# Optimization experiments

Hardware: AMD Instinct MI355X
Metric: run time of the kernel (lower is better)

Reference implementation:

```python
import jax, jax.numpy as jnp
import numpy as np

MARGIN = 0.0
GAP = 0.4
N, D, C = 8192, 128, 10


def setup_inputs() -> dict:
    key = jax.random.key(0)
    k1, k2, k3 = jax.random.split(key, 3)
    inputs = jax.random.normal(k1, (N, D), dtype=jnp.float32)
    pred = jax.random.normal(k2, (N, C), dtype=jnp.float32)
    targets = jax.random.randint(k3, (N,), 0, C, dtype=jnp.int64)
    return {"inputs": inputs, "pred": pred, "targets": targets}


def reference(inputs, pred, targets):
    n = inputs.shape[0]
    # pairwise euclidean distances: ||xi||^2 + ||xj||^2 - 2 xi.xj, clamped + sqrt
    sq = jnp.sum(inputs * inputs, axis=1)                      # [n]
    dist = sq[:, None] + sq[None, :] - 2.0 * (inputs @ inputs.T)
    dist = jnp.sqrt(jnp.clip(dist, 1e-12))                     # [n, n]
    same = targets[:, None] == targets[None, :]                # [n, n] bool

    # confusion detection (original runs under no_grad)
    p = jax.nn.softmax(jax.lax.stop_gradient(pred), axis=1)
    val, top2 = jax.lax.top_k(p, 2)                            # [n,2]
    confuse = (val[:, 0] - val[:, 1] <= GAP) | (top2[:, 0] != targets)  # [n]

    # hard mining per row: hardest positive (max over same-class), hardest negative (min over diff-class)
    dist_ap = jnp.max(jnp.where(same, dist, -jnp.inf), axis=1)  # [n]
    dist_an = jnp.min(jnp.where(same, jnp.inf, dist), axis=1)   # [n]

    # MarginRankingLoss(margin=MARGIN) with y=1: mean(relu(-(an - ap) + margin)) over confused rows
    per_row = jnp.maximum(dist_ap - dist_an + MARGIN, 0.0)
    cnt = jnp.sum(confuse.astype(jnp.float32))
    loss = jnp.sum(jnp.where(confuse, per_row, 0.0)) / jnp.maximum(cnt, 1.0)
    return jnp.where(cnt > 0, loss, 0.0)
```

## Files before the change

### kernel.cpp

```cpp
#include <hip/hip_runtime.h>

#define NROWS 8192
#define DIMX  128
#define KB    192
#define KSEG  12
#define PTB   24576
#define NKS   3
#define NCLS  10
#define GAPV  0.4f
#define DEBIAS 504.03125f
#define SCL   (-0.0078125f)
#define RGR   256
#define NRG   (NROWS / RGR)
#define CHUNK 512
#define NCHUNK (NROWS / CHUNK)
#define NT    (CHUNK / 16)
#define PRW   32

typedef __attribute__((ext_vector_type(4))) int i32x4;

__device__ __forceinline__ int q8(float v) {
  int q = (int)rintf(16.f * v);
  return q > 127 ? 127 : (q < -127 ? -127 : q);
}
__device__ __forceinline__ int pk4(float4 v) {
  return (q8(v.x) & 255) | ((q8(v.y) & 255) << 8) |
         ((q8(v.z) & 255) << 16) | ((q8(v.w) & 255) << 24);
}

__global__ __launch_bounds__(256) void prep_k(const float* __restrict__ x,
                                              const int* __restrict__ tgt,
                                              const float* __restrict__ pred,
                                              char* __restrict__ xa,
                                              char* __restrict__ xbm,
                                              float* __restrict__ sq,
                                              int* __restrict__ conf,
                                              int* __restrict__ emin,
                                              int* __restrict__ emax,
                                              unsigned* __restrict__ ctrs) {
  __shared__ char  pan[8 * PRW * 16];
  __shared__ float ssq[PRW];
  const int tid = threadIdx.x;
  const int blk = blockIdx.x;
  if (blk == 0 && tid < 35) ctrs[tid] = 0u;

  {
    const int r32 = tid >> 3;
    const int sg  = tid & 7;
    const float4* xr = (const float4*)(x + (size_t)(blk * PRW + r32) * DIMX) + sg * 4;
    float ss = 0.f;
    i32x4 w;
    #pragma unroll
    for (int k = 0; k < 4; ++k) {
      const float4 v = xr[k];
      ss += v.x * v.x + v.y * v.y + v.z * v.z + v.w * v.w;
      w[k] = pk4(v);
    }
    *(i32x4*)&pan[(sg * PRW + r32) * 16] = w;
    ss += __shfl_xor(ss, 1, 64);
    ss += __shfl_xor(ss, 2, 64);
    ss += __shfl_xor(ss, 4, 64);
    if (sg == 0) ssq[r32] = ss;
  }
  __syncthreads();

  const int panel = blk >> 2;
  const int rbase = (blk & 3) * PRW;

  {
    const int kseg = tid >> 5;
    const int r32  = tid & 31;
    const i32x4 w = *(const i32x4*)&pan[(kseg * PRW + r32) * 16];
    const size_t off = (size_t)panel * PTB + (size_t)kseg * 2048 + (size_t)(rbase + r32) * 16;
    *(i32x4*)(xa + off)  = w;
    *(i32x4*)(xbm + off) = w;
  }

  if (tid < PRW) {
    const int row = blk * PRW + tid;
    const float s = ssq[tid];
    const int cls = tgt[row];
    const int K  = min((int)rintf(128.f * s), 32385);
    const int t2 = min(K / 127, 254);
    const int b1 = t2 < 127 ? t2 : 127;
    const int b2 = t2 - b1;
    const int rr = min(K - 127 * t2, 126);

    i32x4 a8 = {0,0,0,0}, a9 = {0,0,0,0}, a10 = {0,0,0,0}, z = {0,0,0,0};
    i32x4 b8 = {0,0,0,0}, b9 = {0,0,0,0}, b10 = {0,0,0,0};
    if (cls < 4)      { a8[cls]      = 0x7F7F7F7F; b8[cls]      = (int)0x81818181; }
    else if (cls < 8) { a9[cls - 4]  = 0x7F7F7F7F; b9[cls - 4]  = (int)0x81818181; }
    else              { a10[cls - 8] = 0x7F7F7F7F; b10[cls - 8] = (int)0x81818181; }
    a10[2] = 0x00017F7F;
    b10[2] = ((-b1) & 255) | (((-b2) & 255) << 8) | (((-rr) & 255) << 16);

    char* pa = xa  + (size_t)panel * PTB + (size_t)(rbase + tid) * 16;
    char* pb = xbm + (size_t)panel * PTB + (size_t)(rbase + tid) * 16;
    *(i32x4*)(pa +  8 * 2048) = a8;  *(i32x4*)(pb +  8 * 2048) = b8;
    *(i32x4*)(pa +  9 * 2048) = a9;  *(i32x4*)(pb +  9 * 2048) = b9;
    *(i32x4*)(pa + 10 * 2048) = a10; *(i32x4*)(pb + 10 * 2048) = b10;
    *(i32x4*)(pa + 11 * 2048) = z;   *(i32x4*)(pb + 11 * 2048) = z;

    sq[row]   = s;
    emin[row] = 0x7FFFFFFF;
    emax[row] = (int)0x80000000;

    const float* pp = pred + (size_t)row * NCLS;
    float v[NCLS];
    #pragma unroll
    for (int c = 0; c < NCLS; ++c) v[c] = pp[c];
    float m1 = v[0]; int i1 = 0;
    #pragma unroll
    for (int c = 1; c < NCLS; ++c)
      if (v[c] > m1) { m1 = v[c]; i1 = c; }
    float m2 = -INFINITY, sum = 0.f;
    #pragma unroll
    for (int c = 0; c < NCLS; ++c) {
      sum += __expf(v[c] - m1);
      if (c != i1) m2 = fmaxf(m2, v[c]);
    }
    const float d01 = (1.f - __expf(m2 - m1)) / sum;
    conf[row] = (d01 <= GAPV) || (i1 != cls);
  }
}

__global__ __launch_bounds__(256)
__attribute__((amdgpu_waves_per_eu(2, 8)))
void gram_k(const char* __restrict__ xa,
            const char* __restrict__ xbm,
            const float* __restrict__ sq,
            const int* __restrict__ conf,
            int* __restrict__ emin,
            int* __restrict__ emax,
            unsigned* __restrict__ ctrs,
            float* __restrict__ out) {
  __shared__ unsigned rg_last;
  __shared__ float red[2][4];
  const int tid  = threadIdx.x;
  const int wave = tid >> 6;
  const int lane = tid & 63;
  const int quad = lane >> 4;
  const int m16  = lane & 15;
  const int bx = blockIdx.x, by = blockIdx.y;

  i32x4 A[4][NKS];
  #pragma unroll
  for (int rt = 0; rt < 4; ++rt) {
    const int rbase = wave * 64 + rt * 16;
    const char* pa = xa + (size_t)(bx * 2 + (rbase >> 7)) * PTB
                        + (size_t)((rbase & 127) + m16) * 16;
    #pragma unroll
    for (int ks = 0; ks < NKS; ++ks)
      A[rt][ks] = *(const i32x4*)(pa + (size_t)(ks * 4 + quad) * 2048);
  }
  #pragma unroll
  for (int rt = 0; rt < 4; ++rt)
    #pragma unroll
    for (int ks = 0; ks < NKS; ++ks)
      asm("" : "+v"(A[rt][ks]));

  int Emin[4][4], Emax[4][4];
  #pragma unroll
  for (int r = 0; r < 4; ++r)
    #pragma unroll
    for (int q = 0; q < 4; ++q) { Emin[r][q] = 0x7FFFFFFF; Emax[r][q] = (int)0x80000000; }

  const char* bl = xbm + (size_t)(by * 4) * PTB + (size_t)m16 * 16 + (size_t)quad * 2048;

  i32x4 Bc[NKS], Bn[NKS];
  #pragma unroll
  for (int ks = 0; ks < NKS; ++ks) Bc[ks] = *(const i32x4*)(bl + ks * 8192);

  for (int s = 0; s < NT / 4; ++s) {
    #pragma unroll
    for (int jt = 0; jt < 4; ++jt) {
      const int u  = s * 4 + jt;
      const int un = (u + 1 < NT) ? u + 1 : NT - 1;
      const size_t toff = (size_t)(un >> 3) * PTB + (size_t)(un & 7) * 256;
      #pragma unroll
      for (int ks = 0; ks < NKS; ++ks)
        Bn[ks] = *(const i32x4*)(bl + toff + ks * 8192);

      i32x4 acc[4];
      #pragma unroll
      for (int r = 0; r < 4; ++r) acc[r] = (i32x4){0, 0, 0, 0};
      #pragma unroll
      for (int ks = 0; ks < NKS; ++ks)
        #pragma unroll
        for (int r = 0; r < 4; ++r)
          acc[r] = __builtin_amdgcn_mfma_i32_16x16x64_i8(A[r][ks], Bc[ks], acc[r], 0, 0, 0);

      #pragma unroll
      for (int r = 0; r < 4; ++r)
        #pragma unroll
        for (int q = 0; q < 4; ++q) {
          Emin[r][q] = min(Emin[r][q], acc[r][q]);
          Emax[r][q] = max(Emax[r][q], acc[r][q]);
        }

      #pragma unroll
      for (int ks = 0; ks < NKS; ++ks) Bc[ks] = Bn[ks];
    }
  }

  #pragma unroll
  for (int m = 1; m <= 8; m <<= 1)
    #pragma unroll
    for (int r = 0; r < 4; ++r)
      #pragma unroll
      for (int q = 0; q < 4; ++q) {
        Emin[r][q] = min(Emin[r][q], __shfl_xor(Emin[r][q], m, 64));
        Emax[r][q] = max(Emax[r][q], __shfl_xor(Emax[r][q], m, 64));
      }

  if (m16 == 0) {
    const int rowb = bx * RGR + wave * 64 + quad * 4;
    #pragma unroll
    for (int r = 0; r < 4; ++r)
      #pragma unroll
      for (int q = 0; q < 4; ++q) {
        atomicMin(&emin[rowb + r * 16 + q], Emin[r][q]);
        atomicMax(&emax[rowb + r * 16 + q], Emax[r][q]);
      }
  }

  asm volatile("s_waitcnt vmcnt(0)" ::: "memory");
  __syncthreads();
  if (tid == 0)
    rg_last = (atomicAdd(&ctrs[3 + bx], 1u) == NCHUNK - 1u) ? 1u : 0u;
  __syncthreads();
  if (rg_last) {
    const int row = bx * RGR + tid;
    const int lo = atomicAdd(&emin[row], 0);
    const int hi = atomicAdd(&emax[row], 0);
    float ps = 0.f, pc = 0.f;
    if (conf[row]) {
      const float ap = sqrtf(fmaxf(sq[row] + SCL * (float)lo - DEBIAS, 1e-12f));
      const float an = sqrtf(fmaxf(sq[row] + SCL * (float)hi, 1e-12f));
      ps = fmaxf(ap - an, 0.f);
      pc = 1.f;
    }
    #pragma unroll
    for (int m = 1; m < 64; m <<= 1) {
      ps += __shfl_xor(ps, m, 64);
      pc += __shfl_xor(pc, m, 64);
    }
    if (lane == 0) { red[0][wave] = ps; red[1][wave] = pc; }
    __syncthreads();
    if (tid == 0) {
      float* Ssum = (float*)(ctrs + 1);
      float* Csum = (float*)(ctrs + 2);
      atomicAdd(Ssum, red[0][0] + red[0][1] + red[0][2] + red[0][3]);
      atomicAdd(Csum, red[1][0] + red[1][1] + red[1][2] + red[1][3]);
      asm volatile("s_waitcnt vmcnt(0)" ::: "memory");
      if (atomicAdd(&ctrs[0], 1u) == NRG - 1u) {
        const float St = atomicAdd(Ssum, 0.f);
        const float Ct = atomicAdd(Csum, 0.f);
        out[0] = (Ct > 0.f) ? (St / fmaxf(Ct, 1.f)) : 0.f;
      }
    }
  }
}

extern "C" void kernel_launch(void* const* d_in, const int* in_sizes, int n_in,
                              void* d_out, int out_size, void* d_ws, size_t ws_size,
                              hipStream_t stream) {
  const float* x    = (const float*)d_in[0];
  const float* pred = (const float*)d_in[1];
  const int*   tgt  = (const int*)d_in[2];
  float* out = (float*)d_out;

  char* w = (char*)d_ws;
  const size_t arr_bytes = (size_t)NROWS * KB;
  char*  xa   = w;
  char*  xbm  = w + arr_bytes;
  float* sq   = (float*)(w + 2 * arr_bytes);
  int*   conf = (int*)(w + 2 * arr_bytes + (size_t)NROWS * 4);
  int*   emin = (int*)(w + 2 * arr_bytes + (size_t)NROWS * 8);
  int*   emax = (int*)(w + 2 * arr_bytes + (size_t)NROWS * 12);
  unsigned* ctrs = (unsigned*)(w + 2 * arr_bytes + (size_t)NROWS * 16);

  hipLaunchKernelGGL(prep_k, dim3(NROWS / PRW), dim3(256), 0, stream,
                     x, tgt, pred, xa, xbm, sq, conf, emin, emax, ctrs);
  hipLaunchKernelGGL(gram_k, dim3(NRG, NCHUNK), dim3(256), 0, stream,
                     xa, xbm, sq, conf, emin, emax, ctrs, out);
}
```

Measured before the change: 83.05 us.

## Exploit Gram matrix symmetry with upper-triangular block tiling and column reductions

```diff
diff --git a/kernel.cpp b/kernel.cpp
--- a/kernel.cpp
+++ b/kernel.cpp
@@ -12,9 +12,8 @@
 #define SCL   (-0.0078125f)
 #define RGR   256
 #define NRG   (NROWS / RGR)
-#define CHUNK 512
-#define NCHUNK (NROWS / CHUNK)
-#define NT    (CHUNK / 16)
+#define NT2   16
+#define NBLK2 (NRG * (NRG + 1) / 2)
 #define PRW   32
 
 typedef __attribute__((ext_vector_type(4))) int i32x4;
@@ -91,8 +90,11 @@
     if (cls < 4)      { a8[cls]      = 0x7F7F7F7F; b8[cls]      = (int)0x81818181; }
     else if (cls < 8) { a9[cls - 4]  = 0x7F7F7F7F; b9[cls - 4]  = (int)0x81818181; }
     else              { a10[cls - 8] = 0x7F7F7F7F; b10[cls - 8] = (int)0x81818181; }
-    a10[2] = 0x00017F7F;
-    b10[2] = ((-b1) & 255) | (((-b2) & 255) << 8) | (((-rr) & 255) << 16);
+    a10[2] = 0x00017F7F | (b1 << 24);
+    a10[3] = (b2 & 255) | ((rr & 255) << 8);
+    b10[2] = ((-b1) & 255) | (((-b2) & 255) << 8) |
+             (((-rr) & 255) << 16) | (0x81 << 24);
+    b10[3] = 0x81 | (0xFF << 8);
 
     char* pa = xa  + (size_t)panel * PTB + (size_t)(rbase + tid) * 16;
     char* pb = xbm + (size_t)panel * PTB + (size_t)(rbase + tid) * 16;
@@ -134,20 +136,24 @@
             int* __restrict__ emax,
             unsigned* __restrict__ ctrs,
             float* __restrict__ out) {
-  __shared__ unsigned rg_last;
+  __shared__ unsigned fI, fJ;
   __shared__ float red[2][4];
   const int tid  = threadIdx.x;
   const int wave = tid >> 6;
   const int lane = tid & 63;
   const int quad = lane >> 4;
   const int m16  = lane & 15;
-  const int bx = blockIdx.x, by = blockIdx.y;
+
+  int t = blockIdx.x, I = 0;
+  while (t >= NRG - I) { t -= NRG - I; ++I; }
+  const int J = I + t;
+  const bool diag = (I == J);
 
   i32x4 A[4][NKS];
   #pragma unroll
   for (int rt = 0; rt < 4; ++rt) {
     const int rbase = wave * 64 + rt * 16;
-    const char* pa = xa + (size_t)(bx * 2 + (rbase >> 7)) * PTB
+    const char* pa = xa + (size_t)(I * 2 + (rbase >> 7)) * PTB
                         + (size_t)((rbase & 127) + m16) * 16;
     #pragma unroll
     for (int ks = 0; ks < NKS; ++ks)
@@ -165,17 +171,17 @@
     #pragma unroll
     for (int q = 0; q < 4; ++q) { Emin[r][q] = 0x7FFFFFFF; Emax[r][q] = (int)0x80000000; }
 
-  const char* bl = xbm + (size_t)(by * 4) * PTB + (size_t)m16 * 16 + (size_t)quad * 2048;
+  const char* bl = xbm + (size_t)(J * 2) * PTB + (size_t)m16 * 16 + (size_t)quad * 2048;
 
   i32x4 Bc[NKS], Bn[NKS];
   #pragma unroll
   for (int ks = 0; ks < NKS; ++ks) Bc[ks] = *(const i32x4*)(bl + ks * 8192);
 
-  for (int s = 0; s < NT / 4; ++s) {
+  for (int s = 0; s < NT2 / 4; ++s) {
     #pragma unroll
     for (int jt = 0; jt < 4; ++jt) {
       const int u  = s * 4 + jt;
-      const int un = (u + 1 < NT) ? u + 1 : NT - 1;
+      const int un = (u + 1 < NT2) ? u + 1 : NT2 - 1;
       const size_t toff = (size_t)(un >> 3) * PTB + (size_t)(un & 7) * 256;
       #pragma unroll
       for (int ks = 0; ks < NKS; ++ks)
@@ -198,6 +204,26 @@
           Emax[r][q] = max(Emax[r][q], acc[r][q]);
         }
 
+      if (!diag) {
+        int cmn = acc[0][0], cmx = acc[0][0];
+        #pragma unroll
+        for (int r = 0; r < 4; ++r)
+          #pragma unroll
+          for (int q = 0; q < 4; ++q) {
+            cmn = min(cmn, acc[r][q]);
+            cmx = max(cmx, acc[r][q]);
+          }
+        cmn = min(cmn, __shfl_xor(cmn, 16, 64));
+        cmn = min(cmn, __shfl_xor(cmn, 32, 64));
+        cmx = max(cmx, __shfl_xor(cmx, 16, 64));
+        cmx = max(cmx, __shfl_xor(cmx, 32, 64));
+        if (lane < 16) {
+          const int col = J * RGR + u * 16 + m16;
+          atomicMin(&emin[col], cmn);
+          atomicMax(&emax[col], cmx);
+        }
+      }
+
       #pragma unroll
       for (int ks = 0; ks < NKS; ++ks) Bc[ks] = Bn[ks];
     }
@@ -214,7 +240,7 @@
       }
 
   if (m16 == 0) {
-    const int rowb = bx * RGR + wave * 64 + quad * 4;
+    const int rowb = I * RGR + wave * 64 + quad * 4;
     #pragma unroll
     for (int r = 0; r < 4; ++r)
       #pragma unroll
@@ -226,38 +252,50 @@
 
   asm volatile("s_waitcnt vmcnt(0)" ::: "memory");
   __syncthreads();
-  if (tid == 0)
-    rg_last = (atomicAdd(&ctrs[3 + bx], 1u) == NCHUNK - 1u) ? 1u : 0u;
+  if (tid == 0) {
+    fI = (atomicAdd(&ctrs[3 + I], 1u) == 31u) ? 1u : 0u;
+    fJ = (!diag && atomicAdd(&ctrs[3 + J], 1u) == 31u) ? 1u : 0u;
+  }
   __syncthreads();
-  if (rg_last) {
-    const int row = bx * RGR + tid;
-    const int lo = atomicAdd(&emin[row], 0);
-    const int hi = atomicAdd(&emax[row], 0);
-    float ps = 0.f, pc = 0.f;
-    if (conf[row]) {
-      const float ap = sqrtf(fmaxf(sq[row] + SCL * (float)lo - DEBIAS, 1e-12f));
-      const float an = sqrtf(fmaxf(sq[row] + SCL * (float)hi, 1e-12f));
-      ps = fmaxf(ap - an, 0.f);
-      pc = 1.f;
-    }
-    #pragma unroll
-    for (int m = 1; m < 64; m <<= 1) {
-      ps += __shfl_xor(ps, m, 64);
-      pc += __shfl_xor(pc, m, 64);
-    }
-    if (lane == 0) { red[0][wave] = ps; red[1][wave] = pc; }
-    __syncthreads();
-    if (tid == 0) {
-      float* Ssum = (float*)(ctrs + 1);
-      float* Csum = (float*)(ctrs + 2);
-      atomicAdd(Ssum, red[0][0] + red[0][1] + red[0][2] + red[0][3]);
-      atomicAdd(Csum, red[1][0] + red[1][1] + red[1][2] + red[1][3]);
-      asm volatile("s_waitcnt vmcnt(0)" ::: "memory");
-      if (atomicAdd(&ctrs[0], 1u) == NRG - 1u) {
-        const float St = atomicAdd(Ssum, 0.f);
-        const float Ct = atomicAdd(Csum, 0.f);
-        out[0] = (Ct > 0.f) ? (St / fmaxf(Ct, 1.f)) : 0.f;
-      }
+
+  #pragma unroll 1
+  for (int pass = 0; pass < 2; ++pass) {
+    const unsigned go = pass == 0 ? fI : fJ;
+    const int G = pass == 0 ? I : J;
+    if (go) {
+      const int row = G * RGR + tid;
+      const int lo = atomicAdd(&emin[row], 0);
+      const int hi = atomicAdd(&emax[row], 0);
+      float ps = 0.f, pc = 0.f;
+      if (conf[row]) {
+        const float s = sq[row];
+        const float kf = fminf(rintf(128.f * s), 32385.f);
+        const float ci = fmaf(kf, SCL, s);
+        const float ap = sqrtf(fmaxf(ci + SCL * (float)lo - DEBIAS, 1e-12f));
+        const float an = sqrtf(fmaxf(ci + SCL * (float)hi, 1e-12f));
+        ps = fmaxf(ap - an, 0.f);
+        pc = 1.f;
+      }
+      #pragma unroll
+      for (int m = 1; m < 64; m <<= 1) {
+        ps += __shfl_xor(ps, m, 64);
+        pc += __shfl_xor(pc, m, 64);
+      }
+      if (lane == 0) { red[0][wave] = ps; red[1][wave] = pc; }
+      __syncthreads();
+      if (tid == 0) {
+        float* Ssum = (float*)(ctrs + 1);
+        float* Csum = (float*)(ctrs + 2);
+        atomicAdd(Ssum, red[0][0] + red[0][1] + red[0][2] + red[0][3]);
+        atomicAdd(Csum, red[1][0] + red[1][1] + red[1][2] + red[1][3]);
+        asm volatile("s_waitcnt vmcnt(0)" ::: "memory");
+        if (atomicAdd(&ctrs[0], 1u) == NRG - 1u) {
+          const float St = atomicAdd(Ssum, 0.f);
+          const float Ct = atomicAdd(Csum, 0.f);
+          out[0] = (Ct > 0.f) ? (St / fmaxf(Ct, 1.f)) : 0.f;
+        }
+      }
+      __syncthreads();
     }
   }
 }
@@ -282,6 +320,6 @@
 
   hipLaunchKernelGGL(prep_k, dim3(NROWS / PRW), dim3(256), 0, stream,
                      x, tgt, pred, xa, xbm, sq, conf, emin, emax, ctrs);
-  hipLaunchKernelGGL(gram_k, dim3(NRG, NCHUNK), dim3(256), 0, stream,
+  hipLaunchKernelGGL(gram_k, dim3(NBLK2), dim3(256), 0, stream,
                      xa, xbm, sq, conf, emin, emax, ctrs, out);
 }
```

New measurement: 98.57 us. 18.7% more time.
